# Kernel optimization log

Hardware: AMD Instinct MI355X
Metric: run time of the kernel (lower is better)

## Reference

```python
import jax, jax.numpy as jnp
import numpy as np

N, E, DIN, DOUT = 40000, 640000, 128, 10


def _gat_layer(h_in, src, dst, W, a_src, a_dst, b, n_nodes):
    # h: [N, D]; edges include self-loops already
    h = h_in @ W
    alpha = jax.nn.leaky_relu((h @ a_src)[src] + (h @ a_dst)[dst], 0.2)  # [E']
    m = jax.ops.segment_max(alpha, dst, num_segments=n_nodes)
    e = jnp.exp(alpha - m[dst])
    s = jax.ops.segment_sum(e, dst, num_segments=n_nodes)
    coef = e / (s[dst] + 1e-16)
    out = jax.ops.segment_sum(h[src] * coef[:, None], dst, num_segments=n_nodes)
    return out + b


def setup_inputs() -> dict:
    key = jax.random.key(0)
    ks = jax.random.split(key, 20)
    p = lambda k, shp: (jax.random.normal(k, shp, dtype=jnp.float32) * 0.05)
    inp = {
        "x": jax.random.normal(ks[0], (N, DIN), dtype=jnp.float32),
        "edge_index": jax.random.randint(ks[1], (2, E), 0, N, dtype=jnp.int32),
        "batch": jnp.sort(jax.random.randint(ks[2], (N,), 0, 64, dtype=jnp.int32)),
        "edge_attr": jax.random.normal(ks[3], (E, 4), dtype=jnp.float32),
        # GATConv 1: 128 -> 64
        "W1": p(ks[4], (DIN, 64)), "a1s": p(ks[5], (64,)), "a1d": p(ks[6], (64,)), "b1": jnp.zeros((64,), jnp.float32),
        # GATConv 2: 64 -> 128
        "W2": p(ks[7], (64, 128)), "a2s": p(ks[8], (128,)), "a2d": p(ks[9], (128,)), "b2": jnp.zeros((128,), jnp.float32),
        # GATConv 3: 128 -> 128
        "W3": p(ks[10], (128, 128)), "a3s": p(ks[11], (128,)), "a3d": p(ks[12], (128,)), "b3": jnp.zeros((128,), jnp.float32),
        # SAGPooling scorer: GraphConv(128, 1)
        "wp_rel": p(ks[13], (128, 1)), "wp_root": p(ks[14], (128, 1)), "bp": jnp.zeros((1,), jnp.float32),
        # final Linear(128, out_channels)
        "Wl": p(ks[15], (128, DOUT)), "bl": jnp.zeros((DOUT,), jnp.float32),
    }
    return inp


def reference(x, edge_index, batch, edge_attr,
              W1, a1s, a1d, b1, W2, a2s, a2d, b2, W3, a3s, a3d, b3,
              wp_rel, wp_root, bp, Wl, bl):
    n = x.shape[0]
    src, dst = edge_index[0], edge_index[1]
    # GATConv adds self-loops (edge_attr unused: edge_dim=None)
    loops = jnp.arange(n, dtype=src.dtype)
    src_sl = jnp.concatenate([src, loops])
    dst_sl = jnp.concatenate([dst, loops])

    h = jax.nn.relu(_gat_layer(x, src_sl, dst_sl, W1, a1s, a1d, b1, n))
    h = jax.nn.relu(_gat_layer(h, src_sl, dst_sl, W2, a2s, a2d, b2, n))
    h = jax.nn.relu(_gat_layer(h, src_sl, dst_sl, W3, a3s, a3d, b3, n))

    # SAGPooling(ratio=1): score via GraphConv (no self-loops), tanh gating, all nodes kept
    agg = jax.ops.segment_sum(h[src], dst, num_segments=n)  # [N, 128]
    score = (agg @ wp_rel + h @ wp_root + bp)[:, 0]         # [N]
    h = h * jnp.tanh(score)[:, None]

    # dropout is identity in eval mode
    return jax.nn.relu(h @ Wl + bl)
```

## Files before the change

### kernel.cpp

```cpp
#include <hip/hip_runtime.h>
#include <math.h>

template<int K, int N>
__global__ __launch_bounds__(256) void gemm_tile(
    const float* __restrict__ A, const float* __restrict__ B,
    float* __restrict__ C, int M,
    const float* __restrict__ bias, const float* __restrict__ score, int outN,
    const float* __restrict__ va, const float* __restrict__ vb,
    float* __restrict__ outa, float* __restrict__ outb)
{
    __shared__ float As[64 * K];
    const int tid = threadIdx.x;
    const int base = blockIdx.x * 64;
    for (int idx = tid; idx < 64 * K; idx += 256) {
        int r = idx / K, k = idx - r * K;
        int gr = base + r;
        As[idx] = (gr < M) ? A[(size_t)gr * K + k] : 0.f;
    }
    __syncthreads();
    constexpr int RSTEP = 256 / N;
    constexpr int NR = 64 / RSTEP;
    const int c = tid % N;
    const int r0 = tid / N;
    float acc[NR];
#pragma unroll
    for (int i = 0; i < NR; ++i) acc[i] = 0.f;
    const float4* As4 = reinterpret_cast<const float4*>(As);
    for (int k = 0; k < K; k += 4) {
        float b0 = B[(k + 0) * N + c];
        float b1 = B[(k + 1) * N + c];
        float b2 = B[(k + 2) * N + c];
        float b3 = B[(k + 3) * N + c];
#pragma unroll
        for (int i = 0; i < NR; ++i) {
            float4 a = As4[((r0 + i * RSTEP) * K + k) >> 2];
            acc[i] = fmaf(a.x, b0, acc[i]);
            acc[i] = fmaf(a.y, b1, acc[i]);
            acc[i] = fmaf(a.z, b2, acc[i]);
            acc[i] = fmaf(a.w, b3, acc[i]);
        }
    }
    if (score == nullptr) {
#pragma unroll
        for (int i = 0; i < NR; ++i) {
            int gr = base + r0 + i * RSTEP;
            if (gr < M) C[(size_t)gr * N + c] = acc[i];
        }
    } else {
        if (c < outN) {
#pragma unroll
            for (int i = 0; i < NR; ++i) {
                int gr = base + r0 + i * RSTEP;
                if (gr < M) {
                    float v = tanhf(score[gr]) * acc[i] + bias[c];
                    C[(size_t)gr * outN + c] = fmaxf(v, 0.f);
                }
            }
        }
    }
    if (va != nullptr) {
        const int w = tid >> 6;
        const int lane = tid & 63;
        for (int rr = 0; rr < 16; ++rr) {
            int r = w * 16 + rr;
            int gr = base + r;
            if (gr < M) {
                float sa = 0.f, sb = 0.f;
#pragma unroll
                for (int k = lane; k < K; k += 64) {
                    float av = As[r * K + k];
                    sa = fmaf(av, va[k], sa);
                    sb = fmaf(av, vb[k], sb);
                }
#pragma unroll
                for (int off = 32; off; off >>= 1) {
                    sa += __shfl_xor(sa, off);
                    sb += __shfl_xor(sb, off);
                }
                if (lane == 0) { outa[gr] = sa; outb[gr] = sb; }
            }
        }
    }
}

__global__ __launch_bounds__(256) void zero_deg(int* __restrict__ deg, int n)
{
    int i = blockIdx.x * 256 + threadIdx.x;
    if (i < n) deg[i] = 0;
}

__global__ __launch_bounds__(256) void hist_deg(
    const int* __restrict__ dst, int* __restrict__ deg, int E, int n)
{
    int e = blockIdx.x * 256 + threadIdx.x;
    if (e >= E + n) return;
    int d = (e < E) ? dst[e] : (e - E);
    atomicAdd(deg + d, 1);
}

__global__ __launch_bounds__(256) void scan_local(
    const int* __restrict__ deg, int* __restrict__ row_start, int* __restrict__ blocksum, int n)
{
    __shared__ int s[256];
    const int t = threadIdx.x;
    const int i = blockIdx.x * 256 + t;
    int v = (i < n) ? deg[i] : 0;
    s[t] = v;
    __syncthreads();
#pragma unroll
    for (int off = 1; off < 256; off <<= 1) {
        int u = (t >= off) ? s[t - off] : 0;
        __syncthreads();
        s[t] += u;
        __syncthreads();
    }
    if (i < n) row_start[i] = s[t] - v;
    if (t == 255) blocksum[blockIdx.x] = s[255];
}

__global__ __launch_bounds__(256) void scan_blocks(int* __restrict__ blocksum, int nb)
{
    __shared__ int s[256];
    const int t = threadIdx.x;
    int v = (t < nb) ? blocksum[t] : 0;
    s[t] = v;
    __syncthreads();
#pragma unroll
    for (int off = 1; off < 256; off <<= 1) {
        int u = (t >= off) ? s[t - off] : 0;
        __syncthreads();
        s[t] += u;
        __syncthreads();
    }
    if (t < nb) blocksum[t] = s[t] - v;
}

__global__ __launch_bounds__(256) void scan_add(
    int* __restrict__ row_start, int* __restrict__ cursor,
    const int* __restrict__ blocksum, int n, int total)
{
    const int i = blockIdx.x * 256 + threadIdx.x;
    if (i < n) {
        int v = row_start[i] + blocksum[blockIdx.x];
        row_start[i] = v;
        cursor[i] = v;
    } else if (i == n) {
        row_start[n] = total;
    }
}

__global__ __launch_bounds__(256) void fill_csr(
    const int* __restrict__ src, const int* __restrict__ dst,
    int* __restrict__ cursor, int* __restrict__ csr_src, int E, int n)
{
    int e = blockIdx.x * 256 + threadIdx.x;
    if (e >= E + n) return;
    int s, d;
    if (e < E) { s = src[e]; d = dst[e]; } else { s = d = e - E; }
    int pos = atomicAdd(cursor + d, 1);
    csr_src[pos] = s;
}

template<int D, bool POOL>
__global__ __launch_bounds__(256) void gat_aggregate(
    const int* __restrict__ row_start, const int* __restrict__ csr_src,
    const float* __restrict__ asv, const float* __restrict__ adv,
    const float* __restrict__ h, const float* __restrict__ bias,
    float* __restrict__ out,
    const float* __restrict__ wpr, const float* __restrict__ wpo,
    float* __restrict__ poolA, float* __restrict__ poolB, int n)
{
    __shared__ float lds_e[4][128];
    __shared__ int   lds_i[4][128];
    const int node = (blockIdx.x * 256 + threadIdx.x) >> 6;
    const int lane = threadIdx.x & 63;
    const int w = threadIdx.x >> 6;
    if (node >= n) return;
    const int beg = row_start[node];
    const int deg = row_start[node + 1] - beg;
    const float advv = adv[node];
    const bool fast = (deg <= 128);

    float amax = -INFINITY;
    if (fast) {
        for (int j = lane; j < deg; j += 64) {
            int s = csr_src[beg + j];
            lds_i[w][j] = s;
            float a = asv[s] + advv;
            a = (a >= 0.f) ? a : 0.2f * a;
            lds_e[w][j] = a;
            amax = fmaxf(amax, a);
        }
    } else {
        for (int j = lane; j < deg; j += 64) {
            float a = asv[csr_src[beg + j]] + advv;
            a = (a >= 0.f) ? a : 0.2f * a;
            amax = fmaxf(amax, a);
        }
    }
#pragma unroll
    for (int off = 32; off; off >>= 1) amax = fmaxf(amax, __shfl_xor(amax, off));

    float ssum = 0.f;
    if (fast) {
        for (int j = lane; j < deg; j += 64) {
            float ev = expf(lds_e[w][j] - amax);
            lds_e[w][j] = ev;
            ssum += ev;
        }
    } else {
        for (int j = lane; j < deg; j += 64) {
            float a = asv[csr_src[beg + j]] + advv;
            a = (a >= 0.f) ? a : 0.2f * a;
            ssum += expf(a - amax);
        }
    }
#pragma unroll
    for (int off = 32; off; off >>= 1) ssum += __shfl_xor(ssum, off);
    const float inv = 1.f / (ssum + 1e-16f);

    if constexpr (D == 128) {
        const float2* h2 = reinterpret_cast<const float2*>(h);
        float2 a0 = {0.f, 0.f}, a1 = {0.f, 0.f}, a2 = {0.f, 0.f}, a3 = {0.f, 0.f};
        int j = 0;
        if (fast) {
            for (; j + 4 <= deg; j += 4) {
                int s0 = lds_i[w][j], s1 = lds_i[w][j + 1], s2 = lds_i[w][j + 2], s3 = lds_i[w][j + 3];
                float c0 = lds_e[w][j] * inv, c1 = lds_e[w][j + 1] * inv;
                float c2 = lds_e[w][j + 2] * inv, c3 = lds_e[w][j + 3] * inv;
                float2 v0 = h2[(size_t)s0 * 64 + lane];
                float2 v1 = h2[(size_t)s1 * 64 + lane];
                float2 v2 = h2[(size_t)s2 * 64 + lane];
                float2 v3 = h2[(size_t)s3 * 64 + lane];
                a0.x = fmaf(v0.x, c0, a0.x); a0.y = fmaf(v0.y, c0, a0.y);
                a1.x = fmaf(v1.x, c1, a1.x); a1.y = fmaf(v1.y, c1, a1.y);
                a2.x = fmaf(v2.x, c2, a2.x); a2.y = fmaf(v2.y, c2, a2.y);
                a3.x = fmaf(v3.x, c3, a3.x); a3.y = fmaf(v3.y, c3, a3.y);
            }
            for (; j < deg; ++j) {
                int s = lds_i[w][j];
                float c = lds_e[w][j] * inv;
                float2 v = h2[(size_t)s * 64 + lane];
                a0.x = fmaf(v.x, c, a0.x); a0.y = fmaf(v.y, c, a0.y);
            }
        } else {
            for (; j < deg; ++j) {
                int s = csr_src[beg + j];
                float a = asv[s] + advv;
                a = (a >= 0.f) ? a : 0.2f * a;
                float c = expf(a - amax) * inv;
                float2 v = h2[(size_t)s * 64 + lane];
                a0.x = fmaf(v.x, c, a0.x); a0.y = fmaf(v.y, c, a0.y);
            }
        }
        float2 o;
        o.x = fmaxf(((a0.x + a1.x) + (a2.x + a3.x)) + bias[2 * lane], 0.f);
        o.y = fmaxf(((a0.y + a1.y) + (a2.y + a3.y)) + bias[2 * lane + 1], 0.f);
        reinterpret_cast<float2*>(out)[(size_t)node * 64 + lane] = o;
        if constexpr (POOL) {
            float pa = fmaf(o.x, wpr[2 * lane], o.y * wpr[2 * lane + 1]);
            float pb = fmaf(o.x, wpo[2 * lane], o.y * wpo[2 * lane + 1]);
#pragma unroll
            for (int off = 32; off; off >>= 1) {
                pa += __shfl_xor(pa, off);
                pb += __shfl_xor(pb, off);
            }
            if (lane == 0) { poolA[node] = pa; poolB[node] = pb; }
        }
    } else {
        float a0 = 0.f, a1 = 0.f, a2 = 0.f, a3 = 0.f;
        int j = 0;
        if (fast) {
            for (; j + 4 <= deg; j += 4) {
                int s0 = lds_i[w][j], s1 = lds_i[w][j + 1], s2 = lds_i[w][j + 2], s3 = lds_i[w][j + 3];
                float c0 = lds_e[w][j] * inv, c1 = lds_e[w][j + 1] * inv;
                float c2 = lds_e[w][j + 2] * inv, c3 = lds_e[w][j + 3] * inv;
                a0 = fmaf(h[(size_t)s0 * D + lane], c0, a0);
                a1 = fmaf(h[(size_t)s1 * D + lane], c1, a1);
                a2 = fmaf(h[(size_t)s2 * D + lane], c2, a2);
                a3 = fmaf(h[(size_t)s3 * D + lane], c3, a3);
            }
            for (; j < deg; ++j) {
                a0 = fmaf(h[(size_t)lds_i[w][j] * D + lane], lds_e[w][j] * inv, a0);
            }
        } else {
            for (; j < deg; ++j) {
                int s = csr_src[beg + j];
                float a = asv[s] + advv;
                a = (a >= 0.f) ? a : 0.2f * a;
                float c = expf(a - amax) * inv;
                a0 = fmaf(h[(size_t)s * D + lane], c, a0);
            }
        }
        out[(size_t)node * D + lane] = fmaxf(((a0 + a1) + (a2 + a3)) + bias[lane], 0.f);
    }
}

__global__ __launch_bounds__(256) void score_csr(
    const int* __restrict__ row_start, const int* __restrict__ csr_src,
    const float* __restrict__ ts, const float* __restrict__ td,
    const float* __restrict__ bp, float* __restrict__ score, int n)
{
    int i = blockIdx.x * 256 + threadIdx.x;
    if (i >= n) return;
    int beg = row_start[i], end = row_start[i + 1];
    float s = td[i] + bp[0] - ts[i];
    for (int j = beg; j < end; ++j) s += ts[csr_src[j]];
    score[i] = s;
}

__global__ __launch_bounds__(256) void precompute(
    const float* __restrict__ W1, const float* __restrict__ a1s, const float* __restrict__ a1d,
    const float* __restrict__ W2, const float* __restrict__ a2s, const float* __restrict__ a2d,
    const float* __restrict__ W3, const float* __restrict__ a3s, const float* __restrict__ a3d,
    const float* __restrict__ Wl, const float* __restrict__ bl,
    float* __restrict__ va1, float* __restrict__ vb1,
    float* __restrict__ va2, float* __restrict__ vb2,
    float* __restrict__ va3, float* __restrict__ vb3,
    float* __restrict__ Wlp, float* __restrict__ blp)
{
    int t = blockIdx.x * 256 + threadIdx.x;
    if (t < 128) {
        float sa = 0.f, sb = 0.f;
        for (int j = 0; j < 64; ++j) {
            float w = W1[t * 64 + j];
            sa = fmaf(w, a1s[j], sa); sb = fmaf(w, a1d[j], sb);
        }
        va1[t] = sa; vb1[t] = sb;
    } else if (t < 192) {
        int k = t - 128;
        float sa = 0.f, sb = 0.f;
        for (int j = 0; j < 128; ++j) {
            float w = W2[k * 128 + j];
            sa = fmaf(w, a2s[j], sa); sb = fmaf(w, a2d[j], sb);
        }
        va2[k] = sa; vb2[k] = sb;
    } else if (t < 320) {
        int k = t - 192;
        float sa = 0.f, sb = 0.f;
        for (int j = 0; j < 128; ++j) {
            float w = W3[k * 128 + j];
            sa = fmaf(w, a3s[j], sa); sb = fmaf(w, a3d[j], sb);
        }
        va3[k] = sa; vb3[k] = sb;
    } else if (t < 320 + 2048) {
        int i = t - 320;
        int k = i >> 4, c = i & 15;
        Wlp[i] = (c < 10) ? Wl[k * 10 + c] : 0.f;
    } else if (t < 320 + 2048 + 16) {
        int c = t - (320 + 2048);
        blp[c] = (c < 10) ? bl[c] : 0.f;
    }
}

extern "C" void kernel_launch(void* const* d_in, const int* in_sizes, int n_in,
                              void* d_out, int out_size, void* d_ws, size_t ws_size,
                              hipStream_t stream) {
    const float* x   = (const float*)d_in[0];
    const int*   ei  = (const int*)d_in[1];
    const float* W1  = (const float*)d_in[4];
    const float* a1s = (const float*)d_in[5];
    const float* a1d = (const float*)d_in[6];
    const float* b1  = (const float*)d_in[7];
    const float* W2  = (const float*)d_in[8];
    const float* a2s = (const float*)d_in[9];
    const float* a2d = (const float*)d_in[10];
    const float* b2  = (const float*)d_in[11];
    const float* W3  = (const float*)d_in[12];
    const float* a3s = (const float*)d_in[13];
    const float* a3d = (const float*)d_in[14];
    const float* b3  = (const float*)d_in[15];
    const float* wpr = (const float*)d_in[16];
    const float* wpo = (const float*)d_in[17];
    const float* bp  = (const float*)d_in[18];
    const float* Wl  = (const float*)d_in[19];
    const float* bl  = (const float*)d_in[20];

    const int n = in_sizes[0] / 128;
    const int E = in_sizes[1] / 2;
    const int Esl = E + n;
    const int* src = ei;
    const int* dst = ei + E;

    float* ws = (float*)d_ws;
    const size_t nd = (size_t)n * 128;
    float* bufA      = ws;
    float* bufB      = bufA + nd;
    float* asv       = bufB + nd;
    float* adv       = asv + n;
    float* tsv       = adv + n;
    float* tdv       = tsv + n;
    float* score     = tdv + n;
    int*   deg       = (int*)(score + n);
    int*   row_start = deg + n;
    int*   cursor    = row_start + n + 1;
    int*   blocksum  = cursor + n;
    int*   csr_src   = blocksum + 256;
    float* va1       = (float*)(csr_src + Esl);
    float* vb1       = va1 + 128;
    float* va2       = vb1 + 128;
    float* vb2       = va2 + 64;
    float* va3       = vb2 + 64;
    float* vb3       = va3 + 128;
    float* Wlp       = vb3 + 128;
    float* blp       = Wlp + 128 * 16;

    const unsigned EB = (unsigned)((Esl + 255) / 256);
    const unsigned NB = (unsigned)((n + 255) / 256);
    const unsigned MB = (unsigned)((n + 63) / 64);
    const unsigned WB = (unsigned)(((size_t)n * 64 + 255) / 256);

    precompute<<<10, 256, 0, stream>>>(W1, a1s, a1d, W2, a2s, a2d, W3, a3s, a3d, Wl, bl,
                                       va1, vb1, va2, vb2, va3, vb3, Wlp, blp);
    zero_deg<<<NB, 256, 0, stream>>>(deg, n);
    hist_deg<<<EB, 256, 0, stream>>>(dst, deg, E, n);
    scan_local<<<NB, 256, 0, stream>>>(deg, row_start, blocksum, n);
    scan_blocks<<<1, 256, 0, stream>>>(blocksum, (int)NB);
    scan_add<<<NB, 256, 0, stream>>>(row_start, cursor, blocksum, n, Esl);
    fill_csr<<<EB, 256, 0, stream>>>(src, dst, cursor, csr_src, E, n);

    gemm_tile<128, 64><<<MB, 256, 0, stream>>>(x, W1, bufA, n, nullptr, nullptr, 0, va1, vb1, asv, adv);
    gat_aggregate<64, false><<<WB, 256, 0, stream>>>(row_start, csr_src, asv, adv, bufA, b1, bufB,
                                                     nullptr, nullptr, nullptr, nullptr, n);

    gemm_tile<64, 128><<<MB, 256, 0, stream>>>(bufB, W2, bufA, n, nullptr, nullptr, 0, va2, vb2, asv, adv);
    gat_aggregate<128, false><<<WB, 256, 0, stream>>>(row_start, csr_src, asv, adv, bufA, b2, bufB,
                                                      nullptr, nullptr, nullptr, nullptr, n);

    gemm_tile<128, 128><<<MB, 256, 0, stream>>>(bufB, W3, bufA, n, nullptr, nullptr, 0, va3, vb3, asv, adv);
    gat_aggregate<128, true><<<WB, 256, 0, stream>>>(row_start, csr_src, asv, adv, bufA, b3, bufB,
                                                     wpr, wpo, tsv, tdv, n);

    score_csr<<<NB, 256, 0, stream>>>(row_start, csr_src, tsv, tdv, bp, score, n);
    gemm_tile<128, 16><<<MB, 256, 0, stream>>>(bufB, Wlp, (float*)d_out, n, blp, score, 10,
                                               nullptr, nullptr, nullptr, nullptr);
}
```

Before: 366.6 us.

## Split GEMM columns across grid y, prefetch B rows, fold deg zeroing into precompute

The GEMM kernel gains a column-tile parameter, so the 128-wide output GEMMs launch two blocks per row tile, each handling 64 columns. This doubles parallelism but reloads the A tile into shared memory for each column block. The B row values for the next k step are now loaded before the current FMAs run, to hide their load latency. The separate zero_deg kernel is removed and its zeroing moved into the precompute launch, which now runs NB blocks, saving one kernel launch.

```diff
diff --git a/kernel.cpp b/kernel.cpp
--- a/kernel.cpp
+++ b/kernel.cpp
@@ -1,7 +1,7 @@
 #include <hip/hip_runtime.h>
 #include <math.h>
 
-template<int K, int N>
+template<int K, int N, int NT>
 __global__ __launch_bounds__(256) void gemm_tile(
     const float* __restrict__ A, const float* __restrict__ B,
     float* __restrict__ C, int M,
@@ -9,6 +9,7 @@
     const float* __restrict__ va, const float* __restrict__ vb,
     float* __restrict__ outa, float* __restrict__ outb)
 {
+    static_assert(256 % NT == 0, "NT must divide 256");
     __shared__ float As[64 * K];
     const int tid = threadIdx.x;
     const int base = blockIdx.x * 64;
@@ -18,19 +19,23 @@
         As[idx] = (gr < M) ? A[(size_t)gr * K + k] : 0.f;
     }
     __syncthreads();
-    constexpr int RSTEP = 256 / N;
+    constexpr int RSTEP = 256 / NT;
     constexpr int NR = 64 / RSTEP;
-    const int c = tid % N;
-    const int r0 = tid / N;
+    const int c = tid % NT;
+    const int r0 = tid / NT;
+    const int col = blockIdx.y * NT + c;
     float acc[NR];
 #pragma unroll
     for (int i = 0; i < NR; ++i) acc[i] = 0.f;
     const float4* As4 = reinterpret_cast<const float4*>(As);
+    const float* Bc = B + col;
+    float b0 = Bc[0 * N], b1 = Bc[1 * N], b2 = Bc[2 * N], b3 = Bc[3 * N];
     for (int k = 0; k < K; k += 4) {
-        float b0 = B[(k + 0) * N + c];
-        float b1 = B[(k + 1) * N + c];
-        float b2 = B[(k + 2) * N + c];
-        float b3 = B[(k + 3) * N + c];
+        const int kn = (k + 4 < K) ? (k + 4) : k;
+        float n0 = Bc[(kn + 0) * N];
+        float n1 = Bc[(kn + 1) * N];
+        float n2 = Bc[(kn + 2) * N];
+        float n3 = Bc[(kn + 3) * N];
 #pragma unroll
         for (int i = 0; i < NR; ++i) {
             float4 a = As4[((r0 + i * RSTEP) * K + k) >> 2];
@@ -39,26 +44,27 @@
             acc[i] = fmaf(a.z, b2, acc[i]);
             acc[i] = fmaf(a.w, b3, acc[i]);
         }
+        b0 = n0; b1 = n1; b2 = n2; b3 = n3;
     }
     if (score == nullptr) {
 #pragma unroll
         for (int i = 0; i < NR; ++i) {
             int gr = base + r0 + i * RSTEP;
-            if (gr < M) C[(size_t)gr * N + c] = acc[i];
+            if (gr < M) C[(size_t)gr * N + col] = acc[i];
         }
     } else {
-        if (c < outN) {
+        if (col < outN) {
 #pragma unroll
             for (int i = 0; i < NR; ++i) {
                 int gr = base + r0 + i * RSTEP;
                 if (gr < M) {
-                    float v = tanhf(score[gr]) * acc[i] + bias[c];
-                    C[(size_t)gr * outN + c] = fmaxf(v, 0.f);
+                    float v = tanhf(score[gr]) * acc[i] + bias[col];
+                    C[(size_t)gr * outN + col] = fmaxf(v, 0.f);
                 }
             }
         }
     }
-    if (va != nullptr) {
+    if (va != nullptr && blockIdx.y == 0) {
         const int w = tid >> 6;
         const int lane = tid & 63;
         for (int rr = 0; rr < 16; ++rr) {
@@ -81,12 +87,6 @@
             }
         }
     }
-}
-
-__global__ __launch_bounds__(256) void zero_deg(int* __restrict__ deg, int n)
-{
-    int i = blockIdx.x * 256 + threadIdx.x;
-    if (i < n) deg[i] = 0;
 }
 
 __global__ __launch_bounds__(256) void hist_deg(
@@ -317,9 +317,11 @@
     float* __restrict__ va1, float* __restrict__ vb1,
     float* __restrict__ va2, float* __restrict__ vb2,
     float* __restrict__ va3, float* __restrict__ vb3,
-    float* __restrict__ Wlp, float* __restrict__ blp)
+    float* __restrict__ Wlp, float* __restrict__ blp,
+    int* __restrict__ deg, int n)
 {
     int t = blockIdx.x * 256 + threadIdx.x;
+    if (t < n) deg[t] = 0;
     if (t < 128) {
         float sa = 0.f, sb = 0.f;
         for (int j = 0; j < 64; ++j) {
@@ -410,28 +412,30 @@
     const unsigned MB = (unsigned)((n + 63) / 64);
     const unsigned WB = (unsigned)(((size_t)n * 64 + 255) / 256);
 
-    precompute<<<10, 256, 0, stream>>>(W1, a1s, a1d, W2, a2s, a2d, W3, a3s, a3d, Wl, bl,
-                                       va1, vb1, va2, vb2, va3, vb3, Wlp, blp);
-    zero_deg<<<NB, 256, 0, stream>>>(deg, n);
+    precompute<<<NB, 256, 0, stream>>>(W1, a1s, a1d, W2, a2s, a2d, W3, a3s, a3d, Wl, bl,
+                                       va1, vb1, va2, vb2, va3, vb3, Wlp, blp, deg, n);
     hist_deg<<<EB, 256, 0, stream>>>(dst, deg, E, n);
     scan_local<<<NB, 256, 0, stream>>>(deg, row_start, blocksum, n);
     scan_blocks<<<1, 256, 0, stream>>>(blocksum, (int)NB);
     scan_add<<<NB, 256, 0, stream>>>(row_start, cursor, blocksum, n, Esl);
     fill_csr<<<EB, 256, 0, stream>>>(src, dst, cursor, csr_src, E, n);
 
-    gemm_tile<128, 64><<<MB, 256, 0, stream>>>(x, W1, bufA, n, nullptr, nullptr, 0, va1, vb1, asv, adv);
+    gemm_tile<128, 64, 64><<<dim3(MB, 1), 256, 0, stream>>>(
+        x, W1, bufA, n, nullptr, nullptr, 0, va1, vb1, asv, adv);
     gat_aggregate<64, false><<<WB, 256, 0, stream>>>(row_start, csr_src, asv, adv, bufA, b1, bufB,
                                                      nullptr, nullptr, nullptr, nullptr, n);
 
-    gemm_tile<64, 128><<<MB, 256, 0, stream>>>(bufB, W2, bufA, n, nullptr, nullptr, 0, va2, vb2, asv, adv);
+    gemm_tile<64, 128, 64><<<dim3(MB, 2), 256, 0, stream>>>(
+        bufB, W2, bufA, n, nullptr, nullptr, 0, va2, vb2, asv, adv);
     gat_aggregate<128, false><<<WB, 256, 0, stream>>>(row_start, csr_src, asv, adv, bufA, b2, bufB,
                                                       nullptr, nullptr, nullptr, nullptr, n);
 
-    gemm_tile<128, 128><<<MB, 256, 0, stream>>>(bufB, W3, bufA, n, nullptr, nullptr, 0, va3, vb3, asv, adv);
+    gemm_tile<128, 128, 64><<<dim3(MB, 2), 256, 0, stream>>>(
+        bufB, W3, bufA, n, nullptr, nullptr, 0, va3, vb3, asv, adv);
     gat_aggregate<128, true><<<WB, 256, 0, stream>>>(row_start, csr_src, asv, adv, bufA, b3, bufB,
                                                      wpr, wpo, tsv, tdv, n);
 
     score_csr<<<NB, 256, 0, stream>>>(row_start, csr_src, tsv, tdv, bp, score, n);
-    gemm_tile<128, 16><<<MB, 256, 0, stream>>>(bufB, Wlp, (float*)d_out, n, blp, score, 10,
-                                               nullptr, nullptr, nullptr, nullptr);
-}
+    gemm_tile<128, 16, 16><<<dim3(MB, 1), 256, 0, stream>>>(
+        bufB, Wlp, (float*)d_out, n, blp, score, 10, nullptr, nullptr, nullptr, nullptr);
+}
```

After: 353.9 us. 1.04x faster.
